# Performance work log

Measured on AMD Instinct MI355X. Metric: run time of the kernel, lower is better.

## Reference

```python
import jax, jax.numpy as jnp
import numpy as np


def setup_inputs() -> dict:
    key = jax.random.key(0)
    k1, k2 = jax.random.split(key)
    B, H = 128, 1024
    log_alpha = jax.random.normal(k1, (B, H), dtype=jnp.float32)
    unnormalized_tran = jax.random.normal(k2, (H, H), dtype=jnp.float32)
    return {"log_alpha": log_alpha, "unnormalized_tran": unnormalized_tran}


def reference(log_alpha, unnormalized_tran):
    # tran[i, j] = log P(state j | state i), rows normalized in log space
    tran = jax.nn.log_softmax(unnormalized_tran, axis=-1)  # (H, H)
    # log-domain matmul: out[b, j] = logsumexp_i(log_alpha[b, i] + tran[i, j])
    # broadcast to (B, H, H) then reduce over the source-state axis i
    out = jax.scipy.special.logsumexp(
        log_alpha[:, :, None] + tran[None, :, :], axis=1
    )  # (B, H)
    return out
```

## Files before the change

kernel.cpp:

```cpp
#include <hip/hip_runtime.h>
#include <hip/hip_bf16.h>

#define H 1024
#define B 128

typedef unsigned short u16;
typedef unsigned int u32;
typedef __attribute__((ext_vector_type(8))) short bf16x8;
typedef __attribute__((ext_vector_type(4))) float f32x4;

static __device__ inline u16 f2bf(float x) {
    __hip_bfloat16 h = __float2bfloat16(x);
    return __builtin_bit_cast(u16, h);
}
static __device__ inline u32 pack2(u16 a, u16 b) { return (u32)a | ((u32)b << 16); }

__global__ __launch_bounds__(256) void k1(const float* __restrict__ A,
                                          const float* __restrict__ U,
                                          u16* __restrict__ expUP4,
                                          u16* __restrict__ expA) {
    const int t = threadIdx.x, w = t >> 6, l = t & 63;
    const int blk = blockIdx.x;
    if (blk < 256) {
        __shared__ float part[4][4];
        const int jbase = w * 256 + l;
        float e[4][4];
        float p[4] = {0.f, 0.f, 0.f, 0.f};
        #pragma unroll
        for (int r = 0; r < 4; ++r) {
            const float* Ur = U + (size_t)(blk * 4 + r) * H;
            #pragma unroll
            for (int m = 0; m < 4; ++m) {
                float v = __expf(Ur[jbase + m * 64]);
                e[r][m] = v;
                p[r] += v;
            }
        }
        #pragma unroll
        for (int r = 0; r < 4; ++r)
            #pragma unroll
            for (int off = 32; off > 0; off >>= 1)
                p[r] += __shfl_xor(p[r], off, 64);
        if (l == 0) {
            #pragma unroll
            for (int r = 0; r < 4; ++r) part[r][w] = p[r];
        }
        __syncthreads();
        float is[4];
        #pragma unroll
        for (int r = 0; r < 4; ++r)
            is[r] = 1.0f / (part[r][0] + part[r][1] + part[r][2] + part[r][3]);
        u16* dst = expUP4 + (size_t)blk * H * 4;
        #pragma unroll
        for (int m = 0; m < 4; ++m) {
            const int j = jbase + m * 64;
            uint2 v;
            v.x = pack2(f2bf(e[0][m] * is[0]), f2bf(e[1][m] * is[1]));
            v.y = pack2(f2bf(e[2][m] * is[2]), f2bf(e[3][m] * is[3]));
            *reinterpret_cast<uint2*>(dst + (size_t)j * 4) = v;
        }
    } else {
        const int bb = (blk - 256) * 4;
        #pragma unroll
        for (int r = 0; r < 4; ++r) {
            const float* Ar = A + (size_t)(bb + r) * H;
            u16* Er = expA + (size_t)(bb + r) * H;
            const int j = w * 256 + l * 4;
            float4 a4 = *reinterpret_cast<const float4*>(Ar + j);
            ushort4 o = {f2bf(__expf(a4.x)), f2bf(__expf(a4.y)),
                         f2bf(__expf(a4.z)), f2bf(__expf(a4.w))};
            *reinterpret_cast<ushort4*>(Er + j) = o;
        }
    }
}

__global__ __launch_bounds__(512) void k2(const u16* __restrict__ expA,
                                          const u16* __restrict__ expUP4,
                                          float* __restrict__ out) {
    __shared__ float red[8][4][68];
    const int t = threadIdx.x, l = t & 63, kh = t >> 6;
    const int b0 = blockIdx.x * 16;
    const int j0 = blockIdx.y * 16;
    const int col  = j0 + (l & 15);
    const int arow = b0 + (l & 15);
    const int kg   = l >> 4;

    f32x4 acc = {0.f, 0.f, 0.f, 0.f};
    #pragma unroll
    for (int s = 0; s < 4; ++s) {
        const int kk = kh * 128 + s * 32 + kg * 8;
        bf16x8 af = *reinterpret_cast<const bf16x8*>(expA + (size_t)arow * H + kk);
        const int kq = kk >> 2;
        uint2 g0 = *reinterpret_cast<const uint2*>(expUP4 + ((size_t)kq * H + col) * 4);
        uint2 g1 = *reinterpret_cast<const uint2*>(expUP4 + ((size_t)(kq + 1) * H + col) * 4);
        uint4 bw = {g0.x, g0.y, g1.x, g1.y};
        bf16x8 bfv = __builtin_bit_cast(bf16x8, bw);
        acc = __builtin_amdgcn_mfma_f32_16x16x32_bf16(af, bfv, acc, 0, 0, 0);
    }

    #pragma unroll
    for (int r = 0; r < 4; ++r) red[kh][r][l] = acc[r];
    __syncthreads();

    if (t < 256) {
        const int row = t >> 4, c = t & 15;
        const int kg2 = row >> 2, r = row & 3;
        const int lane = kg2 * 16 + c;
        float v = 0.f;
        #pragma unroll
        for (int k = 0; k < 8; ++k) v += red[k][r][lane];
        out[(size_t)(b0 + row) * H + j0 + c] = __logf(v);
    }
}

extern "C" void kernel_launch(void* const* d_in, const int* in_sizes, int n_in,
                              void* d_out, int out_size, void* d_ws, size_t ws_size,
                              hipStream_t stream) {
    const float* A = (const float*)d_in[0];
    const float* U = (const float*)d_in[1];
    float* out = (float*)d_out;

    char* ws = (char*)d_ws;
    u16* expUP4 = (u16*)ws;
    u16* expA   = (u16*)(ws + (size_t)2 * 1024 * 1024);

    k1<<<288, 256, 0, stream>>>(A, U, expUP4, expA);
    dim3 g(B / 16, H / 16);
    k2<<<g, 512, 0, stream>>>(expA, expUP4, out);
}
```

Baseline: 15.17 us.

## Merge expA work into U blocks, widen k2 tiles, shrink split-K reduction

k1 now runs 256 uniform blocks that each normalize four U rows using float4 loads and 16-byte packed stores, and also convert a 512-element slice of log_alpha. The separate expA blocks are gone. k2 now covers 32 output columns per block with 2 column-halves × 4 K-splits over 8 steps, which halves the grid. Its cross-wave reduction shrinks so that only three waves per half write to LDS while the kh==0 wave sums and takes the log. The goal is to cut block count, load-instruction count and LDS traffic, at the cost of fewer blocks in k2 and more serial MFMA steps per wave.

```diff
diff --git a/kernel.cpp b/kernel.cpp
--- a/kernel.cpp
+++ b/kernel.cpp
@@ -21,74 +21,72 @@
                                           u16* __restrict__ expA) {
     const int t = threadIdx.x, w = t >> 6, l = t & 63;
     const int blk = blockIdx.x;
-    if (blk < 256) {
-        __shared__ float part[4][4];
-        const int jbase = w * 256 + l;
-        float e[4][4];
-        float p[4] = {0.f, 0.f, 0.f, 0.f};
+    __shared__ float part[4][4];
+
+    const int j4 = t * 4;
+    float e[4][4];
+    float p[4];
+    #pragma unroll
+    for (int r = 0; r < 4; ++r) {
+        float4 u4 = *reinterpret_cast<const float4*>(U + (size_t)(blk * 4 + r) * H + j4);
+        e[r][0] = __expf(u4.x); e[r][1] = __expf(u4.y);
+        e[r][2] = __expf(u4.z); e[r][3] = __expf(u4.w);
+        p[r] = e[r][0] + e[r][1] + e[r][2] + e[r][3];
+    }
+    #pragma unroll
+    for (int r = 0; r < 4; ++r)
         #pragma unroll
-        for (int r = 0; r < 4; ++r) {
-            const float* Ur = U + (size_t)(blk * 4 + r) * H;
-            #pragma unroll
-            for (int m = 0; m < 4; ++m) {
-                float v = __expf(Ur[jbase + m * 64]);
-                e[r][m] = v;
-                p[r] += v;
-            }
-        }
+        for (int off = 32; off > 0; off >>= 1)
+            p[r] += __shfl_xor(p[r], off, 64);
+    if (l == 0) {
         #pragma unroll
-        for (int r = 0; r < 4; ++r)
-            #pragma unroll
-            for (int off = 32; off > 0; off >>= 1)
-                p[r] += __shfl_xor(p[r], off, 64);
-        if (l == 0) {
-            #pragma unroll
-            for (int r = 0; r < 4; ++r) part[r][w] = p[r];
-        }
-        __syncthreads();
-        float is[4];
-        #pragma unroll
-        for (int r = 0; r < 4; ++r)
-            is[r] = 1.0f / (part[r][0] + part[r][1] + part[r][2] + part[r][3]);
+        for (int r = 0; r < 4; ++r) part[r][w] = p[r];
+    }
+    __syncthreads();
+    float is[4];
+    #pragma unroll
+    for (int r = 0; r < 4; ++r)
+        is[r] = 1.0f / (part[r][0] + part[r][1] + part[r][2] + part[r][3]);
+
+    {
         u16* dst = expUP4 + (size_t)blk * H * 4;
+        u32 wv[4][2];
         #pragma unroll
         for (int m = 0; m < 4; ++m) {
-            const int j = jbase + m * 64;
-            uint2 v;
-            v.x = pack2(f2bf(e[0][m] * is[0]), f2bf(e[1][m] * is[1]));
-            v.y = pack2(f2bf(e[2][m] * is[2]), f2bf(e[3][m] * is[3]));
-            *reinterpret_cast<uint2*>(dst + (size_t)j * 4) = v;
+            wv[m][0] = pack2(f2bf(e[0][m] * is[0]), f2bf(e[1][m] * is[1]));
+            wv[m][1] = pack2(f2bf(e[2][m] * is[2]), f2bf(e[3][m] * is[3]));
         }
-    } else {
-        const int bb = (blk - 256) * 4;
-        #pragma unroll
-        for (int r = 0; r < 4; ++r) {
-            const float* Ar = A + (size_t)(bb + r) * H;
-            u16* Er = expA + (size_t)(bb + r) * H;
-            const int j = w * 256 + l * 4;
-            float4 a4 = *reinterpret_cast<const float4*>(Ar + j);
-            ushort4 o = {f2bf(__expf(a4.x)), f2bf(__expf(a4.y)),
-                         f2bf(__expf(a4.z)), f2bf(__expf(a4.w))};
-            *reinterpret_cast<ushort4*>(Er + j) = o;
-        }
+        uint4 s0 = {wv[0][0], wv[0][1], wv[1][0], wv[1][1]};
+        uint4 s1 = {wv[2][0], wv[2][1], wv[3][0], wv[3][1]};
+        uint4* ob = reinterpret_cast<uint4*>(dst + (size_t)j4 * 4);
+        ob[0] = s0;
+        ob[1] = s1;
+    }
+
+    {
+        const size_t off = (size_t)blk * 512 + t * 2;
+        float2 a2 = *reinterpret_cast<const float2*>(A + off);
+        ushort2 o = {f2bf(__expf(a2.x)), f2bf(__expf(a2.y))};
+        *reinterpret_cast<ushort2*>(expA + off) = o;
     }
 }
 
 __global__ __launch_bounds__(512) void k2(const u16* __restrict__ expA,
                                           const u16* __restrict__ expUP4,
                                           float* __restrict__ out) {
-    __shared__ float red[8][4][68];
-    const int t = threadIdx.x, l = t & 63, kh = t >> 6;
+    __shared__ float red[3][2][16][16];
+    const int t = threadIdx.x, l = t & 63, w = t >> 6;
+    const int jh = w & 1, kh = w >> 1;
     const int b0 = blockIdx.x * 16;
-    const int j0 = blockIdx.y * 16;
-    const int col  = j0 + (l & 15);
+    const int j0 = blockIdx.y * 32;
+    const int col  = j0 + jh * 16 + (l & 15);
     const int arow = b0 + (l & 15);
     const int kg   = l >> 4;
 
     f32x4 acc = {0.f, 0.f, 0.f, 0.f};
     #pragma unroll
-    for (int s = 0; s < 4; ++s) {
-        const int kk = kh * 128 + s * 32 + kg * 8;
+    for (int s = 0; s < 8; ++s) {
+        const int kk = s * 128 + kh * 32 + kg * 8;
         bf16x8 af = *reinterpret_cast<const bf16x8*>(expA + (size_t)arow * H + kk);
         const int kq = kk >> 2;
         uint2 g0 = *reinterpret_cast<const uint2*>(expUP4 + ((size_t)kq * H + col) * 4);
@@ -98,18 +96,21 @@
         acc = __builtin_amdgcn_mfma_f32_16x16x32_bf16(af, bfv, acc, 0, 0, 0);
     }
 
-    #pragma unroll
-    for (int r = 0; r < 4; ++r) red[kh][r][l] = acc[r];
+    if (kh != 0) {
+        #pragma unroll
+        for (int r = 0; r < 4; ++r)
+            red[kh - 1][jh][(l >> 4) * 4 + r][l & 15] = acc[r];
+    }
     __syncthreads();
-
-    if (t < 256) {
-        const int row = t >> 4, c = t & 15;
-        const int kg2 = row >> 2, r = row & 3;
-        const int lane = kg2 * 16 + c;
-        float v = 0.f;
+    if (kh == 0) {
         #pragma unroll
-        for (int k = 0; k < 8; ++k) v += red[k][r][lane];
-        out[(size_t)(b0 + row) * H + j0 + c] = __logf(v);
+        for (int r = 0; r < 4; ++r) {
+            const int row = (l >> 4) * 4 + r;
+            const float v = acc[r] + red[0][jh][row][l & 15]
+                                   + red[1][jh][row][l & 15]
+                                   + red[2][jh][row][l & 15];
+            out[(size_t)(b0 + row) * H + col] = __logf(v);
+        }
     }
 }
 
@@ -124,7 +125,7 @@
     u16* expUP4 = (u16*)ws;
     u16* expA   = (u16*)(ws + (size_t)2 * 1024 * 1024);
 
-    k1<<<288, 256, 0, stream>>>(A, U, expUP4, expA);
-    dim3 g(B / 16, H / 16);
+    k1<<<256, 256, 0, stream>>>(A, U, expUP4, expA);
+    dim3 g(B / 16, H / 32);
     k2<<<g, 512, 0, stream>>>(expA, expUP4, out);
 }
```

After: 14.76 us. -2.7%, faster.
